# Optimization experiments

Hardware: AMD Instinct MI355X
Metric: run time of the kernel (lower is better)

## Reference

```python
import jax, jax.numpy as jnp
import numpy as np

N, F, B, D = 16384, 256, 48, 8


def setup_inputs() -> dict:
    key = jax.random.key(0)
    k_x, k_e, k_w, k_b = jax.random.split(key, 4)
    x = jax.random.normal(k_x, (N, F), dtype=jnp.float32)
    # per-feature sorted bin boundaries -> left edges and positive widths
    boundaries = jnp.sort(jax.random.uniform(k_e, (F, B + 1), dtype=jnp.float32,
                                             minval=-3.0, maxval=3.0), axis=-1)
    edges = boundaries[:, :-1]                     # [F, B]
    width = jnp.diff(boundaries, axis=-1)          # [F, B], > 0
    bound = 1.0 / np.sqrt(B)                       # nn.Linear default init
    W = jax.random.uniform(k_w, (F, B, D), dtype=jnp.float32, minval=-bound, maxval=bound)
    b = jax.random.uniform(k_b, (F, D), dtype=jnp.float32, minval=-bound, maxval=bound)
    return {"x": x, "edges": edges, "width": width, "W": W, "b": b}


def reference(x, edges, width, W, b):
    # piecewise-linear encoding: [N, F, B]
    h = (x[:, :, None] - edges) / width
    h = jnp.concatenate([
        jnp.minimum(h[..., :1], 1.0),          # first bin: clamp_max(1)
        jnp.clip(h[..., 1:-1], 0.0, 1.0),      # middle bins: clamp(0, 1)
        jnp.maximum(h[..., -1:], 0.0),         # last bin: clamp_min(0)
    ], axis=-1)
    # per-feature tiny Linear(B -> D), then concat over features
    out = jnp.einsum('nfb,fbd->nfd', h, W) + b   # [N, F, D]
    return out.reshape(x.shape[0], -1)           # [N, F*D]
```

## Files before the change

kernel.cpp:

```cpp
#include <hip/hip_runtime.h>


#define NN 16384
#define FF 256
#define BB 48
#define DD 8

#define FT 8
#define NSPLIT 64
#define NPB (NN / NSPLIT)

#define ESTR 52
#define RASTR 100
#define CSTR 396

__global__ __launch_bounds__(256, 8)
void cple_kernel(const float* __restrict__ X,
                 const float* __restrict__ Edg,
                 const float* __restrict__ Wid,
                 const float* __restrict__ W,
                 const float* __restrict__ Bias,
                 float* __restrict__ Out)
{
    __shared__ float sE [FT * ESTR];
    __shared__ float sRA[FT * RASTR];
    __shared__ float sC [FT * CSTR];

    const int tid = threadIdx.x;
    const int f0  = blockIdx.x * FT;
    const int ns  = blockIdx.y;

    if (tid < FT * BB / 4) {
        const float4* E4 = (const float4*)(Edg + (size_t)f0 * BB);
        float4 v = E4[tid];
        int f = tid / 12, j4 = tid % 12;
        *(float4*)&sE[f * ESTR + j4 * 4] = v;
    }
    for (int idx = tid; idx < FT * BB; idx += 256) {
        int f = idx / BB, j = idx - f * BB;
        float e = Edg[(size_t)f0 * BB + idx];
        float w = Wid[(size_t)f0 * BB + idx];
        float r = 1.0f / w;
        sRA[f * RASTR + 2 * j]     = r;
        sRA[f * RASTR + 2 * j + 1] = -e * r;
    }
    {
        const float4* Wt4 = (const float4*)(W + (size_t)f0 * BB * DD);
        #pragma unroll
        for (int q = 0; q < 3; ++q) {
            int idx4 = tid + q * 256;
            float4 v = Wt4[idx4];
            int idx = idx4 * 4;
            int f   = idx / (BB * DD);
            int rem = idx - f * (BB * DD);
            *(float4*)&sC[f * CSTR + DD + rem] = v;
        }
    }
    __syncthreads();

    const int f_l = tid & 7;
    const int n_l = tid >> 3;
    const float* eF  = &sE [f_l * ESTR];
    const float* raF = &sRA[f_l * RASTR];
    const float* cF  = &sC [f_l * CSTR];
    float c4[11];
    #pragma unroll
    for (int m = 0; m < 11; ++m) c4[m] = eF[4 * (m + 1)];

    if (tid < FT * DD) {
        int f = tid >> 3, d = tid & 7;
        float* c = &sC[f * CSTR + d];
        float acc = Bias[(size_t)(f0 + f) * DD + d];
        c[0] = acc;
        #pragma unroll
        for (int ch = 0; ch < 3; ++ch) {
            float w[16];
            #pragma unroll
            for (int j = 0; j < 16; ++j) w[j] = c[(ch * 16 + j + 1) * DD];
            #pragma unroll
            for (int j = 0; j < 16; ++j) { acc += w[j]; c[(ch * 16 + j + 1) * DD] = acc; }
        }
    }
    __syncthreads();

    const float* xp = X + (f0 + f_l);
    float* op = Out + (size_t)(f0 + f_l) * DD;

    int n = ns * NPB + n_l;
    float x = xp[(size_t)n * FF];

    #pragma unroll
    for (int i = 0; i < 8; ++i) {
        float xc = x;
        if (i < 7)
            x = xp[(size_t)(n + 32) * FF];

        int g = 0;
        #pragma unroll
        for (int m = 0; m < 11; ++m) g += (xc >= c4[m]) ? 1 : 0;
        int k4 = g * 4;

        float4 e = *(const float4*)(eF + k4);
        int k = k4 + (xc >= e.y) + (xc >= e.z) + (xc >= e.w);

        float2 ra = *(const float2*)(raF + 2 * k);
        const float* cK = cF + k * DD;
        float4 l0 = *(const float4*)(cK);
        float4 l1 = *(const float4*)(cK + 4);
        float4 h0 = *(const float4*)(cK + 8);
        float4 h1 = *(const float4*)(cK + 12);

        float t = fmaf(xc, ra.x, ra.y);

        float4 o0, o1;
        o0.x = fmaf(t, h0.x - l0.x, l0.x);
        o0.y = fmaf(t, h0.y - l0.y, l0.y);
        o0.z = fmaf(t, h0.z - l0.z, l0.z);
        o0.w = fmaf(t, h0.w - l0.w, l0.w);
        o1.x = fmaf(t, h1.x - l1.x, l1.x);
        o1.y = fmaf(t, h1.y - l1.y, l1.y);
        o1.z = fmaf(t, h1.z - l1.z, l1.z);
        o1.w = fmaf(t, h1.w - l1.w, l1.w);

        float4* o = (float4*)(op + (size_t)n * (FF * DD));
        o[0] = o0;
        o[1] = o1;

        n += 32;
    }
}

extern "C" void kernel_launch(void* const* d_in, const int* in_sizes, int n_in,
                              void* d_out, int out_size, void* d_ws, size_t ws_size,
                              hipStream_t stream) {
    const float* x     = (const float*)d_in[0];
    const float* edges = (const float*)d_in[1];
    const float* width = (const float*)d_in[2];
    const float* W     = (const float*)d_in[3];
    const float* b     = (const float*)d_in[4];
    float* out = (float*)d_out;

    dim3 grid(FF / FT, NSPLIT);
    cple_kernel<<<grid, 256, 0, stream>>>(x, edges, width, W, b, out);
}
```

Measured before the change: 173.6 us.

## Widen feature tile and split output dims across thread pairs

Each block now covers 32 features with 1024 threads instead of 8 features with 256. Each pair of adjacent threads shares one (row, feature) pair, and each thread writes one float4 of the 8 outputs. A wavefront therefore writes a longer contiguous output segment per row and reads a wider contiguous slice of x, which should coalesce global stores and loads better. The first x load is also hoisted above the barrier. In exchange, the bin search is duplicated across both threads of a pair, and shared memory per block grows about fourfold, which may limit blocks per CU.

Measured after the change: 161.4 us (median of 2 runs). -7.1%, faster.

```diff
diff --git a/kernel.cpp b/kernel.cpp
--- a/kernel.cpp
+++ b/kernel.cpp
@@ -6,15 +6,18 @@
 #define BB 48
 #define DD 8
 
-#define FT 8
+#define FT 32
+#define NT 1024
 #define NSPLIT 64
 #define NPB (NN / NSPLIT)
+#define RPI 16
+#define ITERS (NPB / RPI)
 
 #define ESTR 52
 #define RASTR 100
 #define CSTR 396
 
-__global__ __launch_bounds__(256, 8)
+__global__ __launch_bounds__(NT, 8)
 void cple_kernel(const float* __restrict__ X,
                  const float* __restrict__ Edg,
                  const float* __restrict__ Wid,
@@ -36,7 +39,7 @@
         int f = tid / 12, j4 = tid % 12;
         *(float4*)&sE[f * ESTR + j4 * 4] = v;
     }
-    for (int idx = tid; idx < FT * BB; idx += 256) {
+    for (int idx = tid; idx < FT * BB; idx += NT) {
         int f = idx / BB, j = idx - f * BB;
         float e = Edg[(size_t)f0 * BB + idx];
         float w = Wid[(size_t)f0 * BB + idx];
@@ -48,7 +51,7 @@
         const float4* Wt4 = (const float4*)(W + (size_t)f0 * BB * DD);
         #pragma unroll
         for (int q = 0; q < 3; ++q) {
-            int idx4 = tid + q * 256;
+            int idx4 = tid + q * NT;
             float4 v = Wt4[idx4];
             int idx = idx4 * 4;
             int f   = idx / (BB * DD);
@@ -56,13 +59,22 @@
             *(float4*)&sC[f * CSTR + DD + rem] = v;
         }
     }
+
+    const int h   = tid & 1;
+    const int f_l = (tid >> 1) & 31;
+    const int w_l = tid >> 6;
+
+    const float* xp = X + (f0 + f_l);
+    float* op = Out + (size_t)(f0 + f_l) * DD + h * 4;
+
+    const int nbase = ns * NPB + w_l;
+    float xn = xp[(size_t)nbase * FF];
+
     __syncthreads();
 
-    const int f_l = tid & 7;
-    const int n_l = tid >> 3;
     const float* eF  = &sE [f_l * ESTR];
     const float* raF = &sRA[f_l * RASTR];
-    const float* cF  = &sC [f_l * CSTR];
+    const float* cF  = &sC [f_l * CSTR] + h * 4;
     float c4[11];
     #pragma unroll
     for (int m = 0; m < 11; ++m) c4[m] = eF[4 * (m + 1)];
@@ -83,17 +95,12 @@
     }
     __syncthreads();
 
-    const float* xp = X + (f0 + f_l);
-    float* op = Out + (size_t)(f0 + f_l) * DD;
-
-    int n = ns * NPB + n_l;
-    float x = xp[(size_t)n * FF];
-
     #pragma unroll
-    for (int i = 0; i < 8; ++i) {
-        float xc = x;
-        if (i < 7)
-            x = xp[(size_t)(n + 32) * FF];
+    for (int i = 0; i < ITERS; ++i) {
+        int n = nbase + i * RPI;
+        float xc = xn;
+        if (i < ITERS - 1)
+            xn = xp[(size_t)(n + RPI) * FF];
 
         int g = 0;
         #pragma unroll
@@ -105,28 +112,18 @@
 
         float2 ra = *(const float2*)(raF + 2 * k);
         const float* cK = cF + k * DD;
-        float4 l0 = *(const float4*)(cK);
-        float4 l1 = *(const float4*)(cK + 4);
-        float4 h0 = *(const float4*)(cK + 8);
-        float4 h1 = *(const float4*)(cK + 12);
+        float4 lo = *(const float4*)(cK);
+        float4 hi = *(const float4*)(cK + DD);
 
         float t = fmaf(xc, ra.x, ra.y);
 
-        float4 o0, o1;
-        o0.x = fmaf(t, h0.x - l0.x, l0.x);
-        o0.y = fmaf(t, h0.y - l0.y, l0.y);
-        o0.z = fmaf(t, h0.z - l0.z, l0.z);
-        o0.w = fmaf(t, h0.w - l0.w, l0.w);
-        o1.x = fmaf(t, h1.x - l1.x, l1.x);
-        o1.y = fmaf(t, h1.y - l1.y, l1.y);
-        o1.z = fmaf(t, h1.z - l1.z, l1.z);
-        o1.w = fmaf(t, h1.w - l1.w, l1.w);
+        float4 o;
+        o.x = fmaf(t, hi.x - lo.x, lo.x);
+        o.y = fmaf(t, hi.y - lo.y, lo.y);
+        o.z = fmaf(t, hi.z - lo.z, lo.z);
+        o.w = fmaf(t, hi.w - lo.w, lo.w);
 
-        float4* o = (float4*)(op + (size_t)n * (FF * DD));
-        o[0] = o0;
-        o[1] = o1;
-
-        n += 32;
+        *(float4*)(op + (size_t)n * (FF * DD)) = o;
     }
 }
 
@@ -141,5 +138,5 @@
     float* out = (float*)d_out;
 
     dim3 grid(FF / FT, NSPLIT);
-    cple_kernel<<<grid, 256, 0, stream>>>(x, edges, width, W, b, out);
+    cple_kernel<<<grid, NT, 0, stream>>>(x, edges, width, W, b, out);
 }
```
